# Kernel optimization log

Hardware: AMD Instinct MI355X
Metric: run time of the kernel (lower is better)

Reference implementation:

```python
import jax, jax.numpy as jnp
import numpy as np
import math

MAX_DELAY = 25
TAU = 2.0
VTH = 1.0
BN_EPS = 1e-5
ATAN_ALPHA = 2.0


def build_dcls_kernel(W, P, SIG, D):
    # Gaussian-interpolated DCLS kernel ('gauss' version).
    # W, P, SIG: (O, I, K) -> kernel (O, I, D)
    lim = D // 2
    j = jnp.arange(D, dtype=W.dtype)                      # (D,)
    Pc = jnp.clip(P, -lim, lim) + lim                     # (O, I, K)
    sig = jnp.abs(SIG) + 0.27
    g = jnp.exp(-0.5 * ((j - Pc[..., None]) / sig[..., None]) ** 2)  # (O,I,K,D)
    g = g / (g.sum(-1, keepdims=True) + 1e-7)
    return jnp.einsum('oik,oikd->oid', W, g)


def dcls_conv_positive(x, W, P, SIG, D):
    # Dale-positive: abs(weight) before kernel construction; padding=0 (VALID)
    k = build_dcls_kernel(jnp.abs(W), P, SIG, D)
    return jax.lax.conv_general_dilated(
        x, k, window_strides=(1,), padding='VALID',
        dimension_numbers=('NCW', 'OIW', 'NCW'))


def batchnorm_m(x, gamma, beta):
    # spikingjelly layer.BatchNorm1d step_mode='m' on (T, B, C):
    # flattens (T*B) as batch, normalizes per channel (training-mode stats).
    mean = x.mean(axis=(0, 1))
    var = x.var(axis=(0, 1))
    return (x - mean) * jax.lax.rsqrt(var + BN_EPS) * gamma + beta


def lif_multistep(x_seq, tau, v_th):
    # LIFNode, decay_input=False, v_reset=0 (hard reset), detach_reset=True,
    # ATan surrogate. x_seq: (T, B, C).
    inv_tau = jnp.asarray(1.0 / tau, x_seq.dtype)
    def step(v, xt):
        v = v * (1.0 - inv_tau) + xt              # charge (decay_input=False)
        u = v - v_th
        sg = jnp.arctan(0.5 * math.pi * ATAN_ALPHA * u) / math.pi + 0.5
        hard = (u >= 0).astype(xt.dtype)
        spike = sg + jax.lax.stop_gradient(hard - sg)
        v = v * (1.0 - jax.lax.stop_gradient(spike))   # hard reset, detached
        return v, spike
    v0 = jnp.zeros(x_seq.shape[1:], x_seq.dtype)
    _, spikes = jax.lax.scan(step, v0, x_seq)
    return spikes


def setup_inputs() -> dict:
    key = jax.random.key(0)
    ks = jax.random.split(key, 8)
    B, C_in, T = 64, 700, 300
    n_out, n_inh, K = 256, 128, 1
    return {
        'x': jax.random.normal(ks[0], (B, C_in, T), jnp.float32),
        'W_inh': jax.random.normal(ks[1], (n_inh, C_in, K), jnp.float32),
        'P_inh': jax.random.normal(ks[2], (n_inh, C_in, K), jnp.float32),
        'SIG_inh': jax.random.uniform(ks[3], (n_inh, C_in, K), jnp.float32),
        'W_exc': jax.random.normal(ks[4], (n_out, C_in, K), jnp.float32),
        'P_exc': jax.random.normal(ks[5], (n_out, C_in, K), jnp.float32),
        'SIG_exc': jax.random.uniform(ks[6], (n_out, C_in, K), jnp.float32),
        'w_exc_inh': jax.random.uniform(ks[7], (n_out, n_inh), jnp.float32),
        'bn_gamma': jnp.ones((n_inh,), jnp.float32),
        'bn_beta': jnp.zeros((n_inh,), jnp.float32),
    }


def reference(x, W_inh, P_inh, SIG_inh, W_exc, P_exc, SIG_exc, w_exc_inh,
              bn_gamma, bn_beta):
    # inhibitory branch
    in_inhib = dcls_conv_positive(x, W_inh, P_inh, SIG_inh, MAX_DELAY)  # (B,Ci,T')
    in_inhib = jnp.transpose(in_inhib, (2, 0, 1))                       # (T',B,Ci)
    in_inhib = batchnorm_m(in_inhib, bn_gamma, bn_beta)
    spikes = lif_multistep(in_inhib, TAU, VTH)                          # (T',B,Ci)
    out_inhib = jnp.einsum('tbi,oi->tbo', spikes, -jnp.abs(w_exc_inh))
    out_inhib = jnp.transpose(out_inhib, (1, 2, 0))                     # (B,O,T')
    # excitatory branch
    excit = dcls_conv_positive(x, W_exc, P_exc, SIG_exc, MAX_DELAY)     # (B,O,T')
    return excit + out_inhib
```

## Files before the change

### kernel.cpp

```cpp
#include <hip/hip_runtime.h>
#include <math.h>

#define CI   700
#define TIN  300
#define DD   25
#define TOUT 276
#define BB   64
#define OINH 128
#define OEXC 256

#define TROWS 312
#define IPAD  704

typedef __attribute__((ext_vector_type(8))) short short8;
typedef __attribute__((ext_vector_type(4))) float f32x4;
typedef __attribute__((ext_vector_type(8))) unsigned short ushort8v;

static __device__ __forceinline__ unsigned short f2bf(float f) {
    unsigned int u = __float_as_uint(f);
    unsigned int r = (u + 0x7FFFu + ((u >> 16) & 1u)) >> 16;
    return (unsigned short)r;
}
static __device__ __forceinline__ float bf2f(unsigned short h) {
    return __uint_as_float(((unsigned int)h) << 16);
}

static __device__ __forceinline__ void gload_lds16(const void* g, void* l) {
    __builtin_amdgcn_global_load_lds(
        (const __attribute__((address_space(1))) unsigned int*)g,
        (__attribute__((address_space(3))) unsigned int*)l, 16, 0, 0);
}

__global__ void build_kt(const float* __restrict__ W, const float* __restrict__ P,
                         const float* __restrict__ SIG, float* __restrict__ kt, int O) {
    int n = blockIdx.x * 256 + threadIdx.x;
    if (n >= O * CI) return;
    int o = n % O;
    int i = n / O;
    float w   = fabsf(W[o * CI + i]);
    float p   = fminf(fmaxf(P[o * CI + i], -12.f), 12.f) + 12.f;
    float sig = fabsf(SIG[o * CI + i]) + 0.27f;
    float inv = 1.f / sig;
    float g[DD];
    float sum = 0.f;
#pragma unroll
    for (int d = 0; d < DD; ++d) {
        float e = ((float)d - p) * inv;
        g[d] = expf(-0.5f * e * e);
        sum += g[d];
    }
    float sc = w / (sum + 1e-7f);
#pragma unroll
    for (int d = 0; d < DD; ++d)
        kt[(i * DD + d) * O + o] = g[d] * sc;
}

__global__ void kexc_build(const float* __restrict__ W, const float* __restrict__ P,
                           const float* __restrict__ SIG, unsigned short* __restrict__ kb2) {
    int n = blockIdx.x * 256 + threadIdx.x;
    if (n >= OEXC * IPAD) return;
    int o = n / IPAD, ip = n % IPAD;
    if (ip >= CI) {
#pragma unroll
        for (int d = 0; d < DD; ++d)
            kb2[((size_t)d * OEXC + o) * IPAD + ip] = 0;
        return;
    }
    float w   = fabsf(W[o * CI + ip]);
    float p   = fminf(fmaxf(P[o * CI + ip], -12.f), 12.f) + 12.f;
    float sig = fabsf(SIG[o * CI + ip]) + 0.27f;
    float inv = 1.f / sig;
    float g[DD];
    float sum = 0.f;
#pragma unroll
    for (int d = 0; d < DD; ++d) {
        float e = ((float)d - p) * inv;
        g[d] = expf(-0.5f * e * e);
        sum += g[d];
    }
    float sc = w / (sum + 1e-7f);
#pragma unroll
    for (int d = 0; d < DD; ++d)
        kb2[((size_t)d * OEXC + o) * IPAD + ip] = f2bf(g[d] * sc);
}

__global__ void kinh_build(const float* __restrict__ W, const float* __restrict__ P,
                           const float* __restrict__ SIG,
                           unsigned short* __restrict__ kbh, unsigned short* __restrict__ kbl) {
    int n = blockIdx.x * 256 + threadIdx.x;
    if (n >= OINH * IPAD) return;
    int o = n / IPAD, ip = n % IPAD;
    if (ip >= CI) {
#pragma unroll
        for (int d = 0; d < DD; ++d) {
            kbh[((size_t)d * OINH + o) * IPAD + ip] = 0;
            kbl[((size_t)d * OINH + o) * IPAD + ip] = 0;
        }
        return;
    }
    float w   = fabsf(W[o * CI + ip]);
    float p   = fminf(fmaxf(P[o * CI + ip], -12.f), 12.f) + 12.f;
    float sig = fabsf(SIG[o * CI + ip]) + 0.27f;
    float inv = 1.f / sig;
    float g[DD];
    float sum = 0.f;
#pragma unroll
    for (int d = 0; d < DD; ++d) {
        float e = ((float)d - p) * inv;
        g[d] = expf(-0.5f * e * e);
        sum += g[d];
    }
    float sc = w / (sum + 1e-7f);
#pragma unroll
    for (int d = 0; d < DD; ++d) {
        float v = g[d] * sc;
        unsigned short h = f2bf(v);
        kbh[((size_t)d * OINH + o) * IPAD + ip] = h;
        kbl[((size_t)d * OINH + o) * IPAD + ip] = f2bf(v - bf2f(h));
    }
}

__global__ __launch_bounds__(256)
void xt_kernel(const float* __restrict__ x, unsigned short* __restrict__ xTh,
               unsigned short* __restrict__ xTl) {
    __shared__ float tile[64][65];
    const int tid = threadIdx.x;
    const int t0 = blockIdx.x * 64, i0 = blockIdx.y * 64, b = blockIdx.z;
#pragma unroll
    for (int s = 0; s < 16; ++s) {
        int f = s * 256 + tid;
        int tt = f & 63, ii = f >> 6;
        float v = 0.f;
        if (t0 + tt < TIN && i0 + ii < CI)
            v = x[((size_t)b * CI + i0 + ii) * TIN + t0 + tt];
        tile[tt][ii] = v;
    }
    __syncthreads();
#pragma unroll
    for (int s = 0; s < 2; ++s) {
        int f = s * 256 + tid;
        int tt = f >> 3, g = f & 7;
        if (t0 + tt < TROWS) {
            ushort8v vh, vl;
#pragma unroll
            for (int e = 0; e < 8; ++e) {
                float v = tile[tt][g * 8 + e];
                unsigned short h = f2bf(v);
                vh[e] = h;
                vl[e] = f2bf(v - bf2f(h));
            }
            size_t off = ((size_t)b * TROWS + t0 + tt) * IPAD + i0 + g * 8;
            *(ushort8v*)(xTh + off) = vh;
            if (xTl) *(ushort8v*)(xTl + off) = vl;
        }
    }
}

__global__ void wt_kernel(const float* __restrict__ w, float* __restrict__ wt) {
    int n = blockIdx.x * 256 + threadIdx.x;
    if (n >= OINH * OEXC) return;
    int o = n % OEXC, c = n / OEXC;
    wt[c * OEXC + o] = -fabsf(w[o * OINH + c]);
}

__global__ __launch_bounds__(128)
void conv_fused_v3(const unsigned short* __restrict__ xTh, const unsigned short* __restrict__ xTl,
                   const unsigned short* __restrict__ kb2,
                   const unsigned short* __restrict__ kbh, const unsigned short* __restrict__ kbl,
                   float* __restrict__ pexc0, float* __restrict__ pexc1,
                   float* __restrict__ pinh0, float* __restrict__ pinh1) {
    __shared__ unsigned short lds[20480];

    const int tid  = threadIdx.x;
    const int wave = tid >> 6;
    const int lane = tid & 63;
    const int l15 = lane & 15, l4 = lane >> 4;
    const int tt   = blockIdx.x % 3;
    const int ksp  = blockIdx.x / 3;
    const int role = blockIdx.y;
    const int b    = blockIdx.z;
    const int t0   = tt * 96;
    const int icb  = ksp * 11;

    const int ld_r = lane >> 2;
    const int ld_c = (((lane & 3) ^ ((lane >> 3) & 3)) << 4);
    const int SA   = (l15 >> 1) & 3;

    const size_t xstride = (size_t)IPAD * 2;
    const char* xh_base = (const char*)xTh + ((size_t)b * TROWS + t0) * xstride;
    const char* xl_base = (const char*)xTl + ((size_t)b * TROWS + t0) * xstride;

    if (role < 2) {
        unsigned short* xs = lds;
        unsigned short* ks = lds + 4096;
        const int o0 = role * 128 + wave * 64;

        f32x4 acc[4][6];
#pragma unroll
        for (int i = 0; i < 4; ++i)
#pragma unroll
            for (int j = 0; j < 6; ++j) acc[i][j] = (f32x4)0.f;

        for (int c = 0; c < 11; ++c) {
            const size_t cb = (size_t)(icb + c) * 64;
            __syncthreads();
            for (int j = wave; j < 8; j += 2)
                gload_lds16(xh_base + (size_t)(16 * j + ld_r) * xstride + cb + ld_c,
                            (char*)xs + j * 1024);
#pragma unroll
            for (int q = 0; q < 2; ++q) {
                const char* kbase = (const char*)kb2 + ((size_t)(q * OEXC) + o0) * xstride + cb;
                char* kdst = (char*)ks + (q * 2 + wave) * 4096;
#pragma unroll
                for (int j = 0; j < 4; ++j)
                    gload_lds16(kbase + (size_t)(16 * j + ld_r) * xstride + ld_c,
                                kdst + j * 1024);
            }
            asm volatile("s_waitcnt vmcnt(4)" ::: "memory");
            __syncthreads();

            int cur = 0;
            for (int d = 0; d < DD; ++d) {
                if (d < DD - 2) {
                    int nb = cur + 2; if (nb >= 3) nb -= 3;
                    const char* kbase = (const char*)kb2 +
                        ((size_t)((d + 2) * OEXC) + o0) * xstride + cb;
                    char* kdst = (char*)ks + (nb * 2 + wave) * 4096;
#pragma unroll
                    for (int j = 0; j < 4; ++j)
                        gload_lds16(kbase + (size_t)(16 * j + ld_r) * xstride + ld_c,
                                    kdst + j * 1024);
                }
                const char* kp = (const char*)ks + (cur * 2 + wave) * 4096;
                short8 A[4];
#pragma unroll
                for (int i = 0; i < 4; ++i)
                    A[i] = *(const short8*)(kp + (i * 16 + l15) * 64 + ((l4 ^ SA) << 4));
#pragma unroll
                for (int j = 0; j < 6; ++j) {
                    const int tr = j * 16 + l15 + d;
                    short8 Bv = *(const short8*)((const char*)xs + tr * 64 +
                                                 ((l4 ^ ((tr >> 1) & 3)) << 4));
#pragma unroll
                    for (int i = 0; i < 4; ++i)
                        acc[i][j] = __builtin_amdgcn_mfma_f32_16x16x32_bf16(
                            A[i], Bv, acc[i][j], 0, 0, 0);
                }
                if (d < DD - 2)
                    asm volatile("s_waitcnt vmcnt(4)" ::: "memory");
                else if (d == DD - 2)
                    asm volatile("s_waitcnt vmcnt(0)" ::: "memory");
                cur = (cur == 2) ? 0 : cur + 1;
            }
        }
        float* dst = ksp ? pexc1 : pexc0;
#pragma unroll
        for (int i = 0; i < 4; ++i)
#pragma unroll
            for (int j = 0; j < 6; ++j) {
                const int t = t0 + j * 16 + l15;
                if (t < TOUT) {
                    float* op = dst + ((size_t)b * OEXC + o0 + i * 16 + l4 * 4) * TOUT + t;
#pragma unroll
                    for (int r = 0; r < 4; ++r) op[(size_t)r * TOUT] = acc[i][j][r];
                }
            }
    } else {
        unsigned short* xsh = lds;
        unsigned short* xsl = lds + 4096;
        unsigned short* kws = lds + 8192;
        const int o0  = (role - 2) * 64;
        const int o0w = o0 + wave * 32;

        f32x4 acc[2][6];
#pragma unroll
        for (int i = 0; i < 2; ++i)
#pragma unroll
            for (int j = 0; j < 6; ++j) acc[i][j] = (f32x4)0.f;

        for (int c = 0; c < 11; ++c) {
            const size_t cb = (size_t)(icb + c) * 64;
            __syncthreads();
            for (int j = wave; j < 8; j += 2) {
                gload_lds16(xh_base + (size_t)(16 * j + ld_r) * xstride + cb + ld_c,
                            (char*)xsh + j * 1024);
                gload_lds16(xl_base + (size_t)(16 * j + ld_r) * xstride + cb + ld_c,
                            (char*)xsl + j * 1024);
            }
#pragma unroll
            for (int q = 0; q < 2; ++q) {
                const size_t ko = ((size_t)(q * OINH) + o0w) * xstride + cb;
                char* kdst = (char*)kws + (q * 2 + wave) * 4096;
#pragma unroll
                for (int j = 0; j < 2; ++j) {
                    gload_lds16((const char*)kbh + ko + (size_t)(16 * j + ld_r) * xstride + ld_c,
                                kdst + j * 1024);
                    gload_lds16((const char*)kbl + ko + (size_t)(16 * j + ld_r) * xstride + ld_c,
                                kdst + 2048 + j * 1024);
                }
            }
            asm volatile("s_waitcnt vmcnt(4)" ::: "memory");
            __syncthreads();

            int cur = 0;
            for (int d = 0; d < DD; ++d) {
                if (d < DD - 2) {
                    int nb = cur + 2; if (nb >= 3) nb -= 3;
                    const size_t ko = ((size_t)((d + 2) * OINH) + o0w) * xstride + cb;
                    char* kdst = (char*)kws + (nb * 2 + wave) * 4096;
#pragma unroll
                    for (int j = 0; j < 2; ++j) {
                        gload_lds16((const char*)kbh + ko + (size_t)(16 * j + ld_r) * xstride + ld_c,
                                    kdst + j * 1024);
                        gload_lds16((const char*)kbl + ko + (size_t)(16 * j + ld_r) * xstride + ld_c,
                                    kdst + 2048 + j * 1024);
                    }
                }
                const char* kp = (const char*)kws + (cur * 2 + wave) * 4096;
                short8 Ah[2], Al[2];
#pragma unroll
                for (int i = 0; i < 2; ++i) {
                    Ah[i] = *(const short8*)(kp + (i * 16 + l15) * 64 + ((l4 ^ SA) << 4));
                    Al[i] = *(const short8*)(kp + 2048 + (i * 16 + l15) * 64 + ((l4 ^ SA) << 4));
                }
#pragma unroll
                for (int j = 0; j < 6; ++j) {
                    const int tr = j * 16 + l15 + d;
                    const int xo = tr * 64 + ((l4 ^ ((tr >> 1) & 3)) << 4);
                    short8 Bh = *(const short8*)((const char*)xsh + xo);
                    short8 Bl = *(const short8*)((const char*)xsl + xo);
#pragma unroll
                    for (int i = 0; i < 2; ++i) {
                        acc[i][j] = __builtin_amdgcn_mfma_f32_16x16x32_bf16(
                            Ah[i], Bh, acc[i][j], 0, 0, 0);
                        acc[i][j] = __builtin_amdgcn_mfma_f32_16x16x32_bf16(
                            Ah[i], Bl, acc[i][j], 0, 0, 0);
                        acc[i][j] = __builtin_amdgcn_mfma_f32_16x16x32_bf16(
                            Al[i], Bh, acc[i][j], 0, 0, 0);
                    }
                }
                if (d < DD - 2)
                    asm volatile("s_waitcnt vmcnt(4)" ::: "memory");
                else if (d == DD - 2)
                    asm volatile("s_waitcnt vmcnt(0)" ::: "memory");
                cur = (cur == 2) ? 0 : cur + 1;
            }
        }
        float* dst = ksp ? pinh1 : pinh0;
#pragma unroll
        for (int i = 0; i < 2; ++i)
#pragma unroll
            for (int j = 0; j < 6; ++j) {
                const int t = t0 + j * 16 + l15;
                if (t < TOUT) {
                    float* op = dst + ((size_t)b * OINH + o0w + i * 16 + l4 * 4) * TOUT + t;
#pragma unroll
                    for (int r = 0; r < 4; ++r) op[(size_t)r * TOUT] = acc[i][j][r];
                }
            }
    }
}

__global__ void add_exc(const float* __restrict__ p1, float* __restrict__ out) {
    int n = blockIdx.x * 256 + threadIdx.x;
    float4 a = ((const float4*)out)[n];
    float4 v = ((const float4*)p1)[n];
    a.x += v.x; a.y += v.y; a.z += v.z; a.w += v.w;
    ((float4*)out)[n] = a;
}

__global__ void bn_stats2(float* __restrict__ cinh, const float* __restrict__ q1,
                          const float* __restrict__ gamma, const float* __restrict__ beta,
                          float* __restrict__ scale, float* __restrict__ shift) {
    const int c = blockIdx.x, tid = threadIdx.x;
    float sum = 0.f, sq = 0.f;
    for (int idx = tid; idx < BB * TOUT; idx += 256) {
        int b = idx / TOUT, t = idx - b * TOUT;
        size_t off = (size_t)(b * OINH + c) * TOUT + t;
        float v = cinh[off] + q1[off];
        cinh[off] = v;
        sum += v; sq += v * v;
    }
#pragma unroll
    for (int off = 32; off; off >>= 1) {
        sum += __shfl_down(sum, off);
        sq  += __shfl_down(sq, off);
    }
    __shared__ float ls[8];
    int wid = tid >> 6;
    if ((tid & 63) == 0) { ls[wid * 2] = sum; ls[wid * 2 + 1] = sq; }
    __syncthreads();
    if (tid == 0) {
        float S = 0.f, Q = 0.f;
#pragma unroll
        for (int wv = 0; wv < 4; ++wv) { S += ls[wv * 2]; Q += ls[wv * 2 + 1]; }
        const float n = (float)(BB * TOUT);
        float mean = S / n;
        float var  = Q / n - mean * mean;
        float rs   = 1.f / sqrtf(var + 1e-5f);
        float sc   = gamma[c] * rs;
        scale[c] = sc;
        shift[c] = beta[c] - mean * sc;
    }
}

__global__ __launch_bounds__(128)
void lif2(const float* __restrict__ cinh, const float* __restrict__ scale,
          const float* __restrict__ shift, unsigned char* __restrict__ spk) {
    __shared__ float tile[128 * 65];
    const int b = blockIdx.x, c = threadIdx.x;
    const float sc = scale[c], sh = shift[c];
    const float* base = cinh + (size_t)b * OINH * TOUT;
    float v = 0.f;
    for (int tc = 0; tc < TOUT; tc += 64) {
        const int len = (TOUT - tc < 64) ? (TOUT - tc) : 64;
        const int L4 = len >> 2;
        __syncthreads();
        for (int q = c; q < 128 * L4; q += 128) {
            int cc = q / L4, e = q - cc * L4;
            float4 vv = *(const float4*)(base + (size_t)cc * TOUT + tc + e * 4);
            float* dstp = &tile[cc * 65 + e * 4];
            dstp[0] = vv.x; dstp[1] = vv.y; dstp[2] = vv.z; dstp[3] = vv.w;
        }
        __syncthreads();
        for (int t2 = 0; t2 < len; ++t2) {
            float xin = tile[c * 65 + t2] * sc + sh;
            v = 0.5f * v + xin;
            bool s = (v >= 1.f);
            spk[((size_t)(tc + t2) * BB + b) * OINH + c] = s ? 1 : 0;
            v = s ? 0.f : v;
        }
    }
}

__global__ __launch_bounds__(128)
void conv_mfma(const unsigned short* __restrict__ xTh, const unsigned short* __restrict__ kb2,
               float* __restrict__ out) {
    __shared__ unsigned short xs[120 * 64];
    __shared__ unsigned short ks[2][2][64 * 64];

    const int tid  = threadIdx.x;
    const int wave = tid >> 6;
    const int lane = tid & 63;
    const int l15 = lane & 15, l4 = lane >> 4, l7 = lane & 7;
    const int b  = blockIdx.z;
    const int t0 = blockIdx.x * 96;
    const int o0 = blockIdx.y * 128 + wave * 64;

    const int ld_row = lane >> 3;
    const int ld_swz = ((l7 ^ ld_row) << 4);

    f32x4 acc[4][6];
#pragma unroll
    for (int i = 0; i < 4; ++i)
#pragma unroll
        for (int j = 0; j < 6; ++j) acc[i][j] = (f32x4)0.f;

    const char* xrow0 = (const char*)xTh + ((size_t)b * TROWS + t0) * (IPAD * 2);

    for (int ic = 0; ic < 11; ++ic) {
        const int ic0 = ic * 64;
        __syncthreads();
        for (int j = wave; j < 15; j += 2)
            gload_lds16(xrow0 + (size_t)(8 * j + ld_row) * (IPAD * 2) + ic0 * 2 + ld_swz,
                        (char*)xs + j * 1024);
        {
            const char* ksrc = (const char*)kb2 + ((size_t)o0) * (IPAD * 2) + ic0 * 2;
            char* kdst = (char*)ks + (0 * 2 + wave) * 8192;
#pragma unroll
            for (int j = 0; j < 8; ++j)
                gload_lds16(ksrc + (size_t)(8 * j + ld_row) * (IPAD * 2) + ld_swz,
                            kdst + j * 1024);
        }
        asm volatile("s_waitcnt vmcnt(0)" ::: "memory");
        __syncthreads();

        for (int d = 0; d < DD; ++d) {
            const int cur = d & 1;
            if (d < DD - 1) {
                const char* ksrc = (const char*)kb2 +
                    ((size_t)(d + 1) * OEXC + o0) * (IPAD * 2) + ic0 * 2;
                char* kdst = (char*)ks + ((cur ^ 1) * 2 + wave) * 8192;
#pragma unroll
                for (int j = 0; j < 8; ++j)
                    gload_lds16(ksrc + (size_t)(8 * j + ld_row) * (IPAD * 2) + ld_swz,
                                kdst + j * 1024);
            }
            const char* kp = (const char*)ks + (cur * 2 + wave) * 8192;
#pragma unroll
            for (int ks2 = 0; ks2 < 2; ++ks2) {
                const int cg = ks2 * 4 + l4;
                short8 A[4];
#pragma unroll
                for (int i = 0; i < 4; ++i)
                    A[i] = *(const short8*)(kp + (i * 16 + l15) * 128 + ((cg ^ l7) << 4));
#pragma unroll
                for (int j = 0; j < 6; ++j) {
                    const int tr = j * 16 + l15 + d;
                    short8 Bv = *(const short8*)((const char*)xs + tr * 128 +
                                                 ((cg ^ (tr & 7)) << 4));
#pragma unroll
                    for (int i = 0; i < 4; ++i)
                        acc[i][j] = __builtin_amdgcn_mfma_f32_16x16x32_bf16(
                            A[i], Bv, acc[i][j], 0, 0, 0);
                }
            }
            asm volatile("s_waitcnt vmcnt(0)" ::: "memory");
        }
    }

#pragma unroll
    for (int i = 0; i < 4; ++i)
#pragma unroll
        for (int j = 0; j < 6; ++j) {
            const int tt = t0 + j * 16 + l15;
            if (tt < TOUT) {
                float* op = out + ((size_t)b * OEXC + o0 + i * 16 + l4 * 4) * TOUT + tt;
#pragma unroll
                for (int r = 0; r < 4; ++r) op[(size_t)r * TOUT] = acc[i][j][r];
            }
        }
}

__global__ __launch_bounds__(128)
void conv_mfma_inh(const unsigned short* __restrict__ xTh, const unsigned short* __restrict__ xTl,
                   const unsigned short* __restrict__ kbh, const unsigned short* __restrict__ kbl,
                   float* __restrict__ cinh) {
    __shared__ unsigned short xsh[120 * 64];
    __shared__ unsigned short xsl[120 * 64];
    __shared__ unsigned short ksh[2][64 * 64];
    __shared__ unsigned short ksl[2][64 * 64];

    const int tid  = threadIdx.x;
    const int wave = tid >> 6;
    const int lane = tid & 63;
    const int l15 = lane & 15, l4 = lane >> 4, l7 = lane & 7;
    const int b  = blockIdx.z;
    const int t0 = blockIdx.x * 96;
    const int o0 = blockIdx.y * 64;
    const int wtb = wave * 48;

    const int ld_row = lane >> 3;
    const int ld_swz = ((l7 ^ ld_row) << 4);

    f32x4 acc[4][3];
#pragma unroll
    for (int i = 0; i < 4; ++i)
#pragma unroll
        for (int j = 0; j < 3; ++j) acc[i][j] = (f32x4)0.f;

    const char* xrh = (const char*)xTh + ((size_t)b * TROWS + t0) * (IPAD * 2);
    const char* xrl = (const char*)xTl + ((size_t)b * TROWS + t0) * (IPAD * 2);
    const unsigned short* kb = wave ? kbl : kbh;

    for (int ic = 0; ic < 11; ++ic) {
        const int ic0 = ic * 64;
        __syncthreads();
        for (int j = wave; j < 15; j += 2) {
            gload_lds16(xrh + (size_t)(8 * j + ld_row) * (IPAD * 2) + ic0 * 2 + ld_swz,
                        (char*)xsh + j * 1024);
            gload_lds16(xrl + (size_t)(8 * j + ld_row) * (IPAD * 2) + ic0 * 2 + ld_swz,
                        (char*)xsl + j * 1024);
        }
        {
            char* kd = wave ? (char*)ksl[0] : (char*)ksh[0];
#pragma unroll
            for (int j = 0; j < 8; ++j)
                gload_lds16((const char*)kb +
                                ((size_t)(0 * OINH + o0 + 8 * j + ld_row)) * (IPAD * 2) +
                                ic0 * 2 + ld_swz,
                            kd + j * 1024);
        }
        asm volatile("s_waitcnt vmcnt(0)" ::: "memory");
        __syncthreads();

        for (int d = 0; d < DD; ++d) {
            const int cur = d & 1;
            if (d < DD - 1) {
                char* kd = wave ? (char*)ksl[cur ^ 1] : (char*)ksh[cur ^ 1];
#pragma unroll
                for (int j = 0; j < 8; ++j)
                    gload_lds16((const char*)kb +
                                    ((size_t)((d + 1) * OINH + o0 + 8 * j + ld_row)) * (IPAD * 2) +
                                    ic0 * 2 + ld_swz,
                                kd + j * 1024);
            }
            const char* kph = (const char*)ksh[cur];
            const char* kpl = (const char*)ksl[cur];
#pragma unroll
            for (int k2 = 0; k2 < 2; ++k2) {
                const int cg = k2 * 4 + l4;
                short8 Ah[4], Al[4];
#pragma unroll
                for (int i = 0; i < 4; ++i) {
                    Ah[i] = *(const short8*)(kph + (i * 16 + l15) * 128 + ((cg ^ l7) << 4));
                    Al[i] = *(const short8*)(kpl + (i * 16 + l15) * 128 + ((cg ^ l7) << 4));
                }
#pragma unroll
                for (int j = 0; j < 3; ++j) {
                    const int tr = wtb + j * 16 + l15 + d;
                    short8 Bh = *(const short8*)((const char*)xsh + tr * 128 +
                                                 ((cg ^ (tr & 7)) << 4));
                    short8 Bl = *(const short8*)((const char*)xsl + tr * 128 +
                                                 ((cg ^ (tr & 7)) << 4));
#pragma unroll
                    for (int i = 0; i < 4; ++i) {
                        acc[i][j] = __builtin_amdgcn_mfma_f32_16x16x32_bf16(
                            Ah[i], Bh, acc[i][j], 0, 0, 0);
                        acc[i][j] = __builtin_amdgcn_mfma_f32_16x16x32_bf16(
                            Ah[i], Bl, acc[i][j], 0, 0, 0);
                        acc[i][j] = __builtin_amdgcn_mfma_f32_16x16x32_bf16(
                            Al[i], Bh, acc[i][j], 0, 0, 0);
                    }
                }
            }
            asm volatile("s_waitcnt vmcnt(0)" ::: "memory");
            __syncthreads();
        }
    }

#pragma unroll
    for (int i = 0; i < 4; ++i)
#pragma unroll
        for (int j = 0; j < 3; ++j) {
            const int tt = t0 + wtb + j * 16 + l15;
            if (tt < TOUT) {
                float* op = cinh + ((size_t)b * OINH + o0 + i * 16 + l4 * 4) * TOUT + tt;
#pragma unroll
                for (int r = 0; r < 4; ++r) op[(size_t)r * TOUT] = acc[i][j][r];
            }
        }
}

__global__ void bn_stats(const float* __restrict__ cinh, const float* __restrict__ gamma,
                         const float* __restrict__ beta, float* __restrict__ scale,
                         float* __restrict__ shift) {
    const int c = blockIdx.x, tid = threadIdx.x;
    float sum = 0.f, sq = 0.f;
    for (int idx = tid; idx < BB * TOUT; idx += 256) {
        int b = idx / TOUT, t = idx - b * TOUT;
        float v = cinh[(size_t)(b * OINH + c) * TOUT + t];
        sum += v; sq += v * v;
    }
#pragma unroll
    for (int off = 32; off; off >>= 1) {
        sum += __shfl_down(sum, off);
        sq  += __shfl_down(sq, off);
    }
    __shared__ float ls[8];
    int wid = tid >> 6;
    if ((tid & 63) == 0) { ls[wid * 2] = sum; ls[wid * 2 + 1] = sq; }
    __syncthreads();
    if (tid == 0) {
        float S = 0.f, Q = 0.f;
#pragma unroll
        for (int wv = 0; wv < 4; ++wv) { S += ls[wv * 2]; Q += ls[wv * 2 + 1]; }
        const float n = (float)(BB * TOUT);
        float mean = S / n;
        float var  = Q / n - mean * mean;
        float rs   = 1.f / sqrtf(var + 1e-5f);
        float sc   = gamma[c] * rs;
        scale[c] = sc;
        shift[c] = beta[c] - mean * sc;
    }
}

__global__ __launch_bounds__(256)
void finale(const unsigned char* __restrict__ spk, const float* __restrict__ wt,
            float* __restrict__ out) {
    __shared__ float s_lds[64 * 129];
    const int tid = threadIdx.x;
    const int tx = tid & 15, ty = tid >> 4;
    const int b = blockIdx.z, t0 = blockIdx.x * 64, o0 = blockIdx.y * 64;

#pragma unroll
    for (int s = 0; s < 32; ++s) {
        int f = tid + s * 256;
        int tt = f >> 7, c = f & 127;
        float v = 0.f;
        if (t0 + tt < TOUT) v = (float)spk[((size_t)(t0 + tt) * BB + b) * OINH + c];
        s_lds[tt * 129 + c] = v;
    }
    __syncthreads();

    float acc[4][4] = {{0.f}};
#pragma unroll 4
    for (int c = 0; c < 128; ++c) {
        float4 wv = *(const float4*)(wt + c * OEXC + o0 + ty * 4);
        float wvv[4] = {wv.x, wv.y, wv.z, wv.w};
        float sv[4];
#pragma unroll
        for (int rt = 0; rt < 4; ++rt) sv[rt] = s_lds[(tx * 4 + rt) * 129 + c];
#pragma unroll
        for (int ro = 0; ro < 4; ++ro)
#pragma unroll
            for (int rt = 0; rt < 4; ++rt)
                acc[ro][rt] += wvv[ro] * sv[rt];
    }

    const int tvalid = TOUT - t0;
    if (tx * 4 < tvalid) {
#pragma unroll
        for (int ro = 0; ro < 4; ++ro) {
            float* op = out + (size_t)(b * OEXC + o0 + ty * 4 + ro) * TOUT + t0 + tx * 4;
            float4 v = *(float4*)op;
            v.x += acc[ro][0]; v.y += acc[ro][1]; v.z += acc[ro][2]; v.w += acc[ro][3];
            *(float4*)op = v;
        }
    }
}

__global__ void lif_kernel(const float* __restrict__ cinh, const float* __restrict__ scale,
                           const float* __restrict__ shift, unsigned char* __restrict__ spk) {
    const int b = blockIdx.x, c = threadIdx.x;
    const float sc = scale[c], sh = shift[c];
    const float* row = cinh + (size_t)(b * OINH + c) * TOUT;
    float v = 0.f;
    for (int t = 0; t < TOUT; ++t) {
        float xin = row[t] * sc + sh;
        v = 0.5f * v + xin;
        unsigned char s = (v >= 1.f) ? 1 : 0;
        spk[((size_t)t * BB + b) * OINH + c] = s;
        v = (v >= 1.f) ? 0.f : v;
    }
}

extern "C" void kernel_launch(void* const* d_in, const int* in_sizes, int n_in,
                              void* d_out, int out_size, void* d_ws, size_t ws_size,
                              hipStream_t stream) {
    const float* x       = (const float*)d_in[0];
    const float* W_inh   = (const float*)d_in[1];
    const float* P_inh   = (const float*)d_in[2];
    const float* SIG_inh = (const float*)d_in[3];
    const float* W_exc   = (const float*)d_in[4];
    const float* P_exc   = (const float*)d_in[5];
    const float* SIG_exc = (const float*)d_in[6];
    const float* w_ei    = (const float*)d_in[7];
    const float* gamma   = (const float*)d_in[8];
    const float* beta    = (const float*)d_in[9];
    float* out = (float*)d_out;

    const size_t XT_ELEMS   = (size_t)BB * TROWS * IPAD;
    const size_t KEXC_ELEMS = (size_t)DD * OEXC * IPAD;
    const size_t KINH_ELEMS = (size_t)DD * OINH * IPAD;
    const size_t CINH_ELEMS = (size_t)BB * OINH * TOUT;
    const size_t PEXC_ELEMS = (size_t)BB * OEXC * TOUT;

    const size_t NEED_FAST = 2 * XT_ELEMS * 2 + KEXC_ELEMS * 2 + 2 * KINH_ELEMS * 2 +
                             CINH_ELEMS * 4 + OINH * OEXC * 4 + CINH_ELEMS;
    const size_t NEED_FAST2 = (2 * XT_ELEMS + KEXC_ELEMS + 2 * KINH_ELEMS) * 2 +
                              (PEXC_ELEMS + 2 * CINH_ELEMS + OINH * OEXC + 256) * 4 +
                              CINH_ELEMS;

    if (ws_size >= NEED_FAST2) {
        unsigned short* xTh = (unsigned short*)d_ws;
        unsigned short* xTl = xTh + XT_ELEMS;
        unsigned short* kb2 = xTl + XT_ELEMS;
        unsigned short* kbh = kb2 + KEXC_ELEMS;
        unsigned short* kbl = kbh + KINH_ELEMS;
        float* pexc1 = (float*)(kbl + KINH_ELEMS);
        float* cinh  = pexc1 + PEXC_ELEMS;
        float* pinh1 = cinh + CINH_ELEMS;
        float* wt    = pinh1 + CINH_ELEMS;
        float* scale = wt + OINH * OEXC;
        float* shift = scale + OINH;
        unsigned char* spk = (unsigned char*)(shift + OINH);

        hipLaunchKernelGGL(kexc_build, dim3((OEXC * IPAD + 255) / 256), dim3(256), 0, stream,
                           W_exc, P_exc, SIG_exc, kb2);
        hipLaunchKernelGGL(kinh_build, dim3((OINH * IPAD + 255) / 256), dim3(256), 0, stream,
                           W_inh, P_inh, SIG_inh, kbh, kbl);
        hipLaunchKernelGGL(xt_kernel, dim3(5, 11, 64), dim3(256), 0, stream, x, xTh, xTl);
        hipLaunchKernelGGL(wt_kernel, dim3(128), dim3(256), 0, stream, w_ei, wt);

        hipLaunchKernelGGL(conv_fused_v3, dim3(6, 4, 64), dim3(128), 0, stream,
                           xTh, xTl, kb2, kbh, kbl, out, pexc1, cinh, pinh1);

        hipLaunchKernelGGL(add_exc, dim3((unsigned)(PEXC_ELEMS / 4 / 256)), dim3(256), 0, stream,
                           pexc1, out);
        hipLaunchKernelGGL(bn_stats2, dim3(128), dim3(256), 0, stream,
                           cinh, pinh1, gamma, beta, scale, shift);
        hipLaunchKernelGGL(lif2, dim3(64), dim3(128), 0, stream, cinh, scale, shift, spk);
        hipLaunchKernelGGL(finale, dim3(5, 4, 64), dim3(256), 0, stream, spk, wt, out);
    } else if (ws_size >= NEED_FAST) {
        unsigned short* xTh = (unsigned short*)d_ws;
        unsigned short* xTl = xTh + XT_ELEMS;
        unsigned short* kb2 = xTl + XT_ELEMS;
        unsigned short* kbh = kb2 + KEXC_ELEMS;
        unsigned short* kbl = kbh + KINH_ELEMS;
        float* cinh  = (float*)(kbl + KINH_ELEMS);
        float* wt    = cinh + CINH_ELEMS;
        float* scale = wt + OINH * OEXC;
        float* shift = scale + OINH;
        unsigned char* spk = (unsigned char*)(shift + OINH);

        hipLaunchKernelGGL(kexc_build, dim3((OEXC * IPAD + 255) / 256), dim3(256), 0, stream,
                           W_exc, P_exc, SIG_exc, kb2);
        hipLaunchKernelGGL(kinh_build, dim3((OINH * IPAD + 255) / 256), dim3(256), 0, stream,
                           W_inh, P_inh, SIG_inh, kbh, kbl);
        hipLaunchKernelGGL(xt_kernel, dim3(5, 11, 64), dim3(256), 0, stream, x, xTh, xTl);
        hipLaunchKernelGGL(wt_kernel, dim3(128), dim3(256), 0, stream, w_ei, wt);

        hipLaunchKernelGGL(conv_mfma, dim3(3, 2, 64), dim3(128), 0, stream, xTh, kb2, out);
        hipLaunchKernelGGL(conv_mfma_inh, dim3(3, 2, 64), dim3(128), 0, stream,
                           xTh, xTl, kbh, kbl, cinh);

        hipLaunchKernelGGL(bn_stats, dim3(128), dim3(256), 0, stream, cinh, gamma, beta, scale, shift);
        hipLaunchKernelGGL(lif_kernel, dim3(64), dim3(128), 0, stream, cinh, scale, shift, spk);
        hipLaunchKernelGGL(finale, dim3(5, 4, 64), dim3(256), 0, stream, spk, wt, out);
    } else {
        unsigned short* xTh = (unsigned short*)d_ws;
        unsigned short* kb2 = xTh + XT_ELEMS;
        float* kt_inh = (float*)(kb2 + KEXC_ELEMS);
        float* cinh   = kt_inh + 2240000;
        float* wt     = cinh + CINH_ELEMS;
        float* scale  = wt + OINH * OEXC;
        float* shift  = scale + OINH;
        unsigned char* spk = (unsigned char*)(shift + OINH);

        hipLaunchKernelGGL(kexc_build, dim3((OEXC * IPAD + 255) / 256), dim3(256), 0, stream,
                           W_exc, P_exc, SIG_exc, kb2);
        hipLaunchKernelGGL(build_kt, dim3(350), dim3(256), 0, stream,
                           W_inh, P_inh, SIG_inh, kt_inh, OINH);
        hipLaunchKernelGGL(xt_kernel, dim3(5, 11, 64), dim3(256), 0, stream, x, xTh,
                           (unsigned short*)nullptr);
        hipLaunchKernelGGL(wt_kernel, dim3(128), dim3(256), 0, stream, w_ei, wt);

        hipLaunchKernelGGL(conv_mfma, dim3(3, 2, 64), dim3(128), 0, stream, xTh, kb2, out);
        extern __global__ void conv_dcls_fb(const float*, const float*, float*, int);
        hipLaunchKernelGGL(conv_dcls_fb, dim3(5, 1, 64), dim3(256), 0, stream, x, kt_inh, cinh, OINH);

        hipLaunchKernelGGL(bn_stats, dim3(128), dim3(256), 0, stream, cinh, gamma, beta, scale, shift);
        hipLaunchKernelGGL(lif_kernel, dim3(64), dim3(128), 0, stream, cinh, scale, shift, spk);
        hipLaunchKernelGGL(finale, dim3(5, 4, 64), dim3(256), 0, stream, spk, wt, out);
    }
}

__global__ __launch_bounds__(256)
void conv_dcls_fb(const float* __restrict__ x, const float* __restrict__ kt,
                  float* __restrict__ out, int O) {
    __shared__ float k_lds[100 * 128];
    __shared__ float x_lds[4 * 88];

    const int tid = threadIdx.x;
    const int tx = tid & 7;
    const int ty = tid >> 3;
    const int b  = blockIdx.z;
    const int t0 = blockIdx.x * 64;
    const int o0 = blockIdx.y * 128;
    const int tlim = TIN - t0;

    float acc[4][8];
#pragma unroll
    for (int ro = 0; ro < 4; ++ro)
#pragma unroll
        for (int rt = 0; rt < 8; ++rt) acc[ro][rt] = 0.f;

    for (int chunk = 0; chunk < 175; ++chunk) {
        const int i0 = chunk * 4;
        __syncthreads();
#pragma unroll
        for (int s = 0; s < 13; ++s) {
            int f = tid + s * 256;
            if (f < 3200) {
                int j = f >> 5, o4 = f & 31;
                ((float4*)k_lds)[f] =
                    *(const float4*)(kt + (size_t)(i0 * DD + j) * O + o0 + o4 * 4);
            }
        }
        if (tid < 88) {
            int icc = tid / 22, wq = tid % 22;
            float4 v = make_float4(0.f, 0.f, 0.f, 0.f);
            if (wq * 4 < tlim)
                v = *(const float4*)(x + (size_t)(b * CI + i0 + icc) * TIN + t0 + wq * 4);
            ((float4*)x_lds)[tid] = v;
        }
        __syncthreads();
#pragma unroll
        for (int icc = 0; icc < 4; ++icc) {
            float xv[32];
#pragma unroll
            for (int wq = 0; wq < 8; ++wq)
                *(float4*)(xv + 4 * wq) = ((const float4*)(x_lds + icc * 88))[tx * 2 + wq];
#pragma unroll
            for (int d = 0; d < DD; ++d) {
                float4 kv = ((const float4*)(k_lds + (icc * DD + d) * 128))[ty];
                float kvv[4] = {kv.x, kv.y, kv.z, kv.w};
#pragma unroll
                for (int ro = 0; ro < 4; ++ro)
#pragma unroll
                    for (int rt = 0; rt < 8; ++rt)
                        acc[ro][rt] += kvv[ro] * xv[rt + d];
            }
        }
    }
    const int tvalid = TOUT - t0;
#pragma unroll
    for (int ro = 0; ro < 4; ++ro) {
        float* op = out + (size_t)(b * O + o0 + ty * 4 + ro) * TOUT + t0;
#pragma unroll
        for (int u = 0; u < 2; ++u) {
            int toff = tx * 8 + u * 4;
            if (toff < tvalid) {
                float4 v = make_float4(acc[ro][u * 4 + 0], acc[ro][u * 4 + 1],
                                       acc[ro][u * 4 + 2], acc[ro][u * 4 + 3]);
                *(float4*)(op + toff) = v;
            }
        }
    }
}
```

Baseline: 566.2 us.

## Split fused conv across four waves with double-buffered kernel taps

After: 545.3 us. 1.04x faster.

```diff
diff --git a/kernel.cpp b/kernel.cpp
--- a/kernel.cpp
+++ b/kernel.cpp
@@ -163,17 +163,20 @@
     wt[c * OEXC + o] = -fabsf(w[o * OINH + c]);
 }
 
-__global__ __launch_bounds__(128)
-void conv_fused_v3(const unsigned short* __restrict__ xTh, const unsigned short* __restrict__ xTl,
+__global__ __launch_bounds__(256)
+void conv_fused_v6(const unsigned short* __restrict__ xTh, const unsigned short* __restrict__ xTl,
                    const unsigned short* __restrict__ kb2,
                    const unsigned short* __restrict__ kbh, const unsigned short* __restrict__ kbl,
                    float* __restrict__ pexc0, float* __restrict__ pexc1,
                    float* __restrict__ pinh0, float* __restrict__ pinh1) {
-    __shared__ unsigned short lds[20480];
+    __shared__ unsigned short lds[16384];
 
     const int tid  = threadIdx.x;
     const int wave = tid >> 6;
     const int lane = tid & 63;
+    const int wo   = wave & 1;
+    const int wt2  = wave >> 1;
+    const int wtb  = wt2 * 48;
     const int l15 = lane & 15, l4 = lane >> 4;
     const int tt   = blockIdx.x % 3;
     const int ksp  = blockIdx.x / 3;
@@ -193,52 +196,51 @@
     if (role < 2) {
         unsigned short* xs = lds;
         unsigned short* ks = lds + 4096;
-        const int o0 = role * 128 + wave * 64;
-
-        f32x4 acc[4][6];
+        const int o0 = role * 128;
+        const int o0w = o0 + wo * 64;
+
+        f32x4 acc[4][3];
 #pragma unroll
         for (int i = 0; i < 4; ++i)
 #pragma unroll
-            for (int j = 0; j < 6; ++j) acc[i][j] = (f32x4)0.f;
+            for (int j = 0; j < 3; ++j) acc[i][j] = (f32x4)0.f;
 
         for (int c = 0; c < 11; ++c) {
             const size_t cb = (size_t)(icb + c) * 64;
             __syncthreads();
-            for (int j = wave; j < 8; j += 2)
+            for (int j = wave; j < 8; j += 4)
                 gload_lds16(xh_base + (size_t)(16 * j + ld_r) * xstride + cb + ld_c,
                             (char*)xs + j * 1024);
-#pragma unroll
-            for (int q = 0; q < 2; ++q) {
-                const char* kbase = (const char*)kb2 + ((size_t)(q * OEXC) + o0) * xstride + cb;
-                char* kdst = (char*)ks + (q * 2 + wave) * 4096;
+            {
+                const char* kbase = (const char*)kb2 + (size_t)o0w * xstride + cb;
+                char* kdst = (char*)(ks + (0 * 2 + wo) * 2048);
 #pragma unroll
                 for (int j = 0; j < 4; ++j)
                     gload_lds16(kbase + (size_t)(16 * j + ld_r) * xstride + ld_c,
                                 kdst + j * 1024);
             }
-            asm volatile("s_waitcnt vmcnt(4)" ::: "memory");
+            asm volatile("s_waitcnt vmcnt(0)" ::: "memory");
             __syncthreads();
 
-            int cur = 0;
             for (int d = 0; d < DD; ++d) {
-                if (d < DD - 2) {
-                    int nb = cur + 2; if (nb >= 3) nb -= 3;
+                const int cur = d & 1;
+                if (d < DD - 1) {
                     const char* kbase = (const char*)kb2 +
-                        ((size_t)((d + 2) * OEXC) + o0) * xstride + cb;
-                    char* kdst = (char*)ks + (nb * 2 + wave) * 4096;
+                        ((size_t)((d + 1) * OEXC) + o0w) * xstride + cb;
+                    char* kdst = (char*)(ks + ((cur ^ 1) * 2 + wo) * 2048);
 #pragma unroll
                     for (int j = 0; j < 4; ++j)
                         gload_lds16(kbase + (size_t)(16 * j + ld_r) * xstride + ld_c,
                                     kdst + j * 1024);
                 }
-                const char* kp = (const char*)ks + (cur * 2 + wave) * 4096;
+                const char* kp = (const char*)(ks + (cur * 2 + wo) * 2048);
                 short8 A[4];
 #pragma unroll
                 for (int i = 0; i < 4; ++i)
                     A[i] = *(const short8*)(kp + (i * 16 + l15) * 64 + ((l4 ^ SA) << 4));
 #pragma unroll
-                for (int j = 0; j < 6; ++j) {
-                    const int tr = j * 16 + l15 + d;
+                for (int j = 0; j < 3; ++j) {
+                    const int tr = wtb + j * 16 + l15 + d;
                     short8 Bv = *(const short8*)((const char*)xs + tr * 64 +
                                                  ((l4 ^ ((tr >> 1) & 3)) << 4));
 #pragma unroll
@@ -246,21 +248,18 @@
                         acc[i][j] = __builtin_amdgcn_mfma_f32_16x16x32_bf16(
                             A[i], Bv, acc[i][j], 0, 0, 0);
                 }
-                if (d < DD - 2)
-                    asm volatile("s_waitcnt vmcnt(4)" ::: "memory");
-                else if (d == DD - 2)
-                    asm volatile("s_waitcnt vmcnt(0)" ::: "memory");
-                cur = (cur == 2) ? 0 : cur + 1;
+                asm volatile("s_waitcnt vmcnt(0)" ::: "memory");
+                __syncthreads();
             }
         }
         float* dst = ksp ? pexc1 : pexc0;
 #pragma unroll
         for (int i = 0; i < 4; ++i)
 #pragma unroll
-            for (int j = 0; j < 6; ++j) {
-                const int t = t0 + j * 16 + l15;
+            for (int j = 0; j < 3; ++j) {
+                const int t = t0 + wtb + j * 16 + l15;
                 if (t < TOUT) {
-                    float* op = dst + ((size_t)b * OEXC + o0 + i * 16 + l4 * 4) * TOUT + t;
+                    float* op = dst + ((size_t)b * OEXC + o0w + i * 16 + l4 * 4) * TOUT + t;
 #pragma unroll
                     for (int r = 0; r < 4; ++r) op[(size_t)r * TOUT] = acc[i][j][r];
                 }
@@ -270,27 +269,26 @@
         unsigned short* xsl = lds + 4096;
         unsigned short* kws = lds + 8192;
         const int o0  = (role - 2) * 64;
-        const int o0w = o0 + wave * 32;
-
-        f32x4 acc[2][6];
+        const int o0w = o0 + wo * 32;
+
+        f32x4 acc[2][3];
 #pragma unroll
         for (int i = 0; i < 2; ++i)
 #pragma unroll
-            for (int j = 0; j < 6; ++j) acc[i][j] = (f32x4)0.f;
+            for (int j = 0; j < 3; ++j) acc[i][j] = (f32x4)0.f;
 
         for (int c = 0; c < 11; ++c) {
             const size_t cb = (size_t)(icb + c) * 64;
             __syncthreads();
-            for (int j = wave; j < 8; j += 2) {
+            for (int j = wave; j < 8; j += 4) {
                 gload_lds16(xh_base + (size_t)(16 * j + ld_r) * xstride + cb + ld_c,
                             (char*)xsh + j * 1024);
                 gload_lds16(xl_base + (size_t)(16 * j + ld_r) * xstride + cb + ld_c,
                             (char*)xsl + j * 1024);
             }
-#pragma unroll
-            for (int q = 0; q < 2; ++q) {
-                const size_t ko = ((size_t)(q * OINH) + o0w) * xstride + cb;
-                char* kdst = (char*)kws + (q * 2 + wave) * 4096;
+            {
+                const size_t ko = (size_t)o0w * xstride + cb;
+                char* kdst = (char*)(kws + (0 * 2 + wo) * 2048);
 #pragma unroll
                 for (int j = 0; j < 2; ++j) {
                     gload_lds16((const char*)kbh + ko + (size_t)(16 * j + ld_r) * xstride + ld_c,
@@ -299,15 +297,14 @@
                                 kdst + 2048 + j * 1024);
                 }
             }
-            asm volatile("s_waitcnt vmcnt(4)" ::: "memory");
+            asm volatile("s_waitcnt vmcnt(0)" ::: "memory");
             __syncthreads();
 
-            int cur = 0;
             for (int d = 0; d < DD; ++d) {
-                if (d < DD - 2) {
-                    int nb = cur + 2; if (nb >= 3) nb -= 3;
-                    const size_t ko = ((size_t)((d + 2) * OINH) + o0w) * xstride + cb;
-                    char* kdst = (char*)kws + (nb * 2 + wave) * 4096;
+                const int cur = d & 1;
+                if (d < DD - 1) {
+                    const size_t ko = ((size_t)((d + 1) * OINH) + o0w) * xstride + cb;
+                    char* kdst = (char*)(kws + ((cur ^ 1) * 2 + wo) * 2048);
 #pragma unroll
                     for (int j = 0; j < 2; ++j) {
                         gload_lds16((const char*)kbh + ko + (size_t)(16 * j + ld_r) * xstride + ld_c,
@@ -316,7 +313,7 @@
                                     kdst + 2048 + j * 1024);
                     }
                 }
-                const char* kp = (const char*)kws + (cur * 2 + wave) * 4096;
+                const char* kp = (const char*)(kws + (cur * 2 + wo) * 2048);
                 short8 Ah[2], Al[2];
 #pragma unroll
                 for (int i = 0; i < 2; ++i) {
@@ -324,8 +321,8 @@
                     Al[i] = *(const short8*)(kp + 2048 + (i * 16 + l15) * 64 + ((l4 ^ SA) << 4));
                 }
 #pragma unroll
-                for (int j = 0; j < 6; ++j) {
-                    const int tr = j * 16 + l15 + d;
+                for (int j = 0; j < 3; ++j) {
+                    const int tr = wtb + j * 16 + l15 + d;
                     const int xo = tr * 64 + ((l4 ^ ((tr >> 1) & 3)) << 4);
                     short8 Bh = *(const short8*)((const char*)xsh + xo);
                     short8 Bl = *(const short8*)((const char*)xsl + xo);
@@ -339,19 +336,16 @@
                             Al[i], Bh, acc[i][j], 0, 0, 0);
                     }
                 }
-                if (d < DD - 2)
-                    asm volatile("s_waitcnt vmcnt(4)" ::: "memory");
-                else if (d == DD - 2)
-                    asm volatile("s_waitcnt vmcnt(0)" ::: "memory");
-                cur = (cur == 2) ? 0 : cur + 1;
+                asm volatile("s_waitcnt vmcnt(0)" ::: "memory");
+                __syncthreads();
             }
         }
         float* dst = ksp ? pinh1 : pinh0;
 #pragma unroll
         for (int i = 0; i < 2; ++i)
 #pragma unroll
-            for (int j = 0; j < 6; ++j) {
-                const int t = t0 + j * 16 + l15;
+            for (int j = 0; j < 3; ++j) {
+                const int t = t0 + wtb + j * 16 + l15;
                 if (t < TOUT) {
                     float* op = dst + ((size_t)b * OINH + o0w + i * 16 + l4 * 4) * TOUT + t;
 #pragma unroll
@@ -632,6 +626,80 @@
         }
 }
 
+__global__ __launch_bounds__(256)
+void conv_dcls_fb(const float* __restrict__ x, const float* __restrict__ kt,
+                  float* __restrict__ out, int O) {
+    __shared__ float k_lds[100 * 128];
+    __shared__ float x_lds[4 * 88];
+
+    const int tid = threadIdx.x;
+    const int tx = tid & 7;
+    const int ty = tid >> 3;
+    const int b  = blockIdx.z;
+    const int t0 = blockIdx.x * 64;
+    const int o0 = blockIdx.y * 128;
+    const int tlim = TIN - t0;
+
+    float acc[4][8];
+#pragma unroll
+    for (int ro = 0; ro < 4; ++ro)
+#pragma unroll
+        for (int rt = 0; rt < 8; ++rt) acc[ro][rt] = 0.f;
+
+    for (int chunk = 0; chunk < 175; ++chunk) {
+        const int i0 = chunk * 4;
+        __syncthreads();
+#pragma unroll
+        for (int s = 0; s < 13; ++s) {
+            int f = tid + s * 256;
+            if (f < 3200) {
+                int j = f >> 5, o4 = f & 31;
+                ((float4*)k_lds)[f] =
+                    *(const float4*)(kt + (size_t)(i0 * DD + j) * O + o0 + o4 * 4);
+            }
+        }
+        if (tid < 88) {
+            int icc = tid / 22, wq = tid % 22;
+            float4 v = make_float4(0.f, 0.f, 0.f, 0.f);
+            if (wq * 4 < tlim)
+                v = *(const float4*)(x + (size_t)(b * CI + i0 + icc) * TIN + t0 + wq * 4);
+            ((float4*)x_lds)[tid] = v;
+        }
+        __syncthreads();
+#pragma unroll
+        for (int icc = 0; icc < 4; ++icc) {
+            float xv[32];
+#pragma unroll
+            for (int wq = 0; wq < 8; ++wq)
+                *(float4*)(xv + 4 * wq) = ((const float4*)(x_lds + icc * 88))[tx * 2 + wq];
+#pragma unroll
+            for (int d = 0; d < DD; ++d) {
+                float4 kv = ((const float4*)(k_lds + (icc * DD + d) * 128))[ty];
+                float kvv[4] = {kv.x, kv.y, kv.z, kv.w};
+#pragma unroll
+                for (int ro = 0; ro < 4; ++ro)
+#pragma unroll
+                    for (int rt = 0; rt < 8; ++rt)
+                        acc[ro][rt] += kvv[ro] * xv[rt + d];
+            }
+        }
+    }
+    const int tvalid = TOUT - t0;
+#pragma unroll
+    for (int ro = 0; ro < 4; ++ro) {
+        float* op = out + (size_t)(b * O + o0 + ty * 4 + ro) * TOUT + t0;
+#pragma unroll
+        for (int u = 0; u < 2; ++u) {
+            int toff = tx * 8 + u * 4;
+            if (toff < tvalid) {
+                float4 v = make_float4(acc[ro][u * 4 + 0], acc[ro][u * 4 + 1],
+                                       acc[ro][u * 4 + 2], acc[ro][u * 4 + 3]);
+                *(float4*)(op + toff) = v;
+            }
+        }
+    }
+}
+
 __global__ void bn_stats(const float* __restrict__ cinh, const float* __restrict__ gamma,
                          const float* __restrict__ beta, float* __restrict__ scale,
                          float* __restrict__ shift) {
@@ -662,51 +730,6 @@
         float sc   = gamma[c] * rs;
         scale[c] = sc;
         shift[c] = beta[c] - mean * sc;
-    }
-}
-
-__global__ __launch_bounds__(256)
-void finale(const unsigned char* __restrict__ spk, const float* __restrict__ wt,
-            float* __restrict__ out) {
-    __shared__ float s_lds[64 * 129];
-    const int tid = threadIdx.x;
-    const int tx = tid & 15, ty = tid >> 4;
-    const int b = blockIdx.z, t0 = blockIdx.x * 64, o0 = blockIdx.y * 64;
-
-#pragma unroll
-    for (int s = 0; s < 32; ++s) {
-        int f = tid + s * 256;
-        int tt = f >> 7, c = f & 127;
-        float v = 0.f;
-        if (t0 + tt < TOUT) v = (float)spk[((size_t)(t0 + tt) * BB + b) * OINH + c];
-        s_lds[tt * 129 + c] = v;
-    }
-    __syncthreads();
-
-    float acc[4][4] = {{0.f}};
-#pragma unroll 4
-    for (int c = 0; c < 128; ++c) {
-        float4 wv = *(const float4*)(wt + c * OEXC + o0 + ty * 4);
-        float wvv[4] = {wv.x, wv.y, wv.z, wv.w};
-        float sv[4];
-#pragma unroll
-        for (int rt = 0; rt < 4; ++rt) sv[rt] = s_lds[(tx * 4 + rt) * 129 + c];
-#pragma unroll
-        for (int ro = 0; ro < 4; ++ro)
-#pragma unroll
-            for (int rt = 0; rt < 4; ++rt)
-                acc[ro][rt] += wvv[ro] * sv[rt];
-    }
-
-    const int tvalid = TOUT - t0;
-    if (tx * 4 < tvalid) {
-#pragma unroll
-        for (int ro = 0; ro < 4; ++ro) {
-            float* op = out + (size_t)(b * OEXC + o0 + ty * 4 + ro) * TOUT + t0 + tx * 4;
-            float4 v = *(float4*)op;
-            v.x += acc[ro][0]; v.y += acc[ro][1]; v.z += acc[ro][2]; v.w += acc[ro][3];
-            *(float4*)op = v;
-        }
     }
 }
 
@@ -722,6 +745,51 @@
         unsigned char s = (v >= 1.f) ? 1 : 0;
         spk[((size_t)t * BB + b) * OINH + c] = s;
         v = (v >= 1.f) ? 0.f : v;
+    }
+}
+
+__global__ __launch_bounds__(256)
+void finale(const unsigned char* __restrict__ spk, const float* __restrict__ wt,
+            float* __restrict__ out) {
+    __shared__ float s_lds[64 * 129];
+    const int tid = threadIdx.x;
+    const int tx = tid & 15, ty = tid >> 4;
+    const int b = blockIdx.z, t0 = blockIdx.x * 64, o0 = blockIdx.y * 64;
+
+#pragma unroll
+    for (int s = 0; s < 32; ++s) {
+        int f = tid + s * 256;
+        int tt = f >> 7, c = f & 127;
+        float v = 0.f;
+        if (t0 + tt < TOUT) v = (float)spk[((size_t)(t0 + tt) * BB + b) * OINH + c];
+        s_lds[tt * 129 + c] = v;
+    }
+    __syncthreads();
+
+    float acc[4][4] = {{0.f}};
+#pragma unroll 4
+    for (int c = 0; c < 128; ++c) {
+        float4 wv = *(const float4*)(wt + c * OEXC + o0 + ty * 4);
+        float wvv[4] = {wv.x, wv.y, wv.z, wv.w};
+        float sv[4];
+#pragma unroll
+        for (int rt = 0; rt < 4; ++rt) sv[rt] = s_lds[(tx * 4 + rt) * 129 + c];
+#pragma unroll
+        for (int ro = 0; ro < 4; ++ro)
+#pragma unroll
+            for (int rt = 0; rt < 4; ++rt)
+                acc[ro][rt] += wvv[ro] * sv[rt];
+    }
+
+    const int tvalid = TOUT - t0;
+    if (tx * 4 < tvalid) {
+#pragma unroll
+        for (int ro = 0; ro < 4; ++ro) {
+            float* op = out + (size_t)(b * OEXC + o0 + ty * 4 + ro) * TOUT + t0 + tx * 4;
+            float4 v = *(float4*)op;
+            v.x += acc[ro][0]; v.y += acc[ro][1]; v.z += acc[ro][2]; v.w += acc[ro][3];
+            *(float4*)op = v;
+        }
     }
 }
 
@@ -773,7 +841,7 @@
         hipLaunchKernelGGL(xt_kernel, dim3(5, 11, 64), dim3(256), 0, stream, x, xTh, xTl);
         hipLaunchKernelGGL(wt_kernel, dim3(128), dim3(256), 0, stream, w_ei, wt);
 
-        hipLaunchKernelGGL(conv_fused_v3, dim3(6, 4, 64), dim3(128), 0, stream,
+        hipLaunchKernelGGL(conv_fused_v6, dim3(6, 4, 64), dim3(256), 0, stream,
                            xTh, xTl, kb2, kbh, kbl, out, pexc1, cinh, pinh1);
 
         hipLaunchKernelGGL(add_exc, dim3((unsigned)(PEXC_ELEMS / 4 / 256)), dim3(256), 0, stream,
@@ -827,7 +895,6 @@
         hipLaunchKernelGGL(wt_kernel, dim3(128), dim3(256), 0, stream, w_ei, wt);
 
         hipLaunchKernelGGL(conv_mfma, dim3(3, 2, 64), dim3(128), 0, stream, xTh, kb2, out);
-        extern __global__ void conv_dcls_fb(const float*, const float*, float*, int);
         hipLaunchKernelGGL(conv_dcls_fb, dim3(5, 1, 64), dim3(256), 0, stream, x, kt_inh, cinh, OINH);
 
         hipLaunchKernelGGL(bn_stats, dim3(128), dim3(256), 0, stream, cinh, gamma, beta, scale, shift);
@@ -835,77 +902,3 @@
         hipLaunchKernelGGL(finale, dim3(5, 4, 64), dim3(256), 0, stream, spk, wt, out);
     }
 }
-
-__global__ __launch_bounds__(256)
-void conv_dcls_fb(const float* __restrict__ x, const float* __restrict__ kt,
-                  float* __restrict__ out, int O) {
-    __shared__ float k_lds[100 * 128];
-    __shared__ float x_lds[4 * 88];
-
-    const int tid = threadIdx.x;
-    const int tx = tid & 7;
-    const int ty = tid >> 3;
-    const int b  = blockIdx.z;
-    const int t0 = blockIdx.x * 64;
-    const int o0 = blockIdx.y * 128;
-    const int tlim = TIN - t0;
-
-    float acc[4][8];
-#pragma unroll
-    for (int ro = 0; ro < 4; ++ro)
-#pragma unroll
-        for (int rt = 0; rt < 8; ++rt) acc[ro][rt] = 0.f;
-
-    for (int chunk = 0; chunk < 175; ++chunk) {
-        const int i0 = chunk * 4;
-        __syncthreads();
-#pragma unroll
-        for (int s = 0; s < 13; ++s) {
-            int f = tid + s * 256;
-            if (f < 3200) {
-                int j = f >> 5, o4 = f & 31;
-                ((float4*)k_lds)[f] =
-                    *(const float4*)(kt + (size_t)(i0 * DD + j) * O + o0 + o4 * 4);
-            }
-        }
-        if (tid < 88) {
-            int icc = tid / 22, wq = tid % 22;
-            float4 v = make_float4(0.f, 0.f, 0.f, 0.f);
-            if (wq * 4 < tlim)
-                v = *(const float4*)(x + (size_t)(b * CI + i0 + icc) * TIN + t0 + wq * 4);
-            ((float4*)x_lds)[tid] = v;
-        }
-        __syncthreads();
-#pragma unroll
-        for (int icc = 0; icc < 4; ++icc) {
-            float xv[32];
-#pragma unroll
-            for (int wq = 0; wq < 8; ++wq)
-                *(float4*)(xv + 4 * wq) = ((const float4*)(x_lds + icc * 88))[tx * 2 + wq];
-#pragma unroll
-            for (int d = 0; d < DD; ++d) {
-                float4 kv = ((const float4*)(k_lds + (icc * DD + d) * 128))[ty];
-                float kvv[4] = {kv.x, kv.y, kv.z, kv.w};
-#pragma unroll
-                for (int ro = 0; ro < 4; ++ro)
-#pragma unroll
-                    for (int rt = 0; rt < 8; ++rt)
-                        acc[ro][rt] += kvv[ro] * xv[rt + d];
-            }
-        }
-    }
-    const int tvalid = TOUT - t0;
-#pragma unroll
-    for (int ro = 0; ro < 4; ++ro) {
-        float* op = out + (size_t)(b * O + o0 + ty * 4 + ro) * TOUT + t0;
-#pragma unroll
-        for (int u = 0; u < 2; ++u) {
-            int toff = tx * 8 + u * 4;
-            if (toff < tvalid) {
-                float4 v = make_float4(acc[ro][u * 4 + 0], acc[ro][u * 4 + 1],
-                                       acc[ro][u * 4 + 2], acc[ro][u * 4 + 3]);
-                *(float4*)(op + toff) = v;
-            }
-        }
-    }
-}
```
